# Optimization experiments

Measured on AMD Instinct MI355X. Metric: run time of the kernel, lower is better.

Reference implementation:

```python
import jax, jax.numpy as jnp
import numpy as np

N_NODES = 100000
N_EDGES = 1600000
F_IN, F1, F2, F3 = 128, 128, 128, 64


def setup_inputs() -> dict:
    key = jax.random.key(0)
    ks = jax.random.split(key, 10)
    edge_index = jax.random.randint(ks[0], (2, N_EDGES), 0, N_NODES, dtype=jnp.int64)
    x = jax.random.normal(ks[1], (N_NODES, F_IN), dtype=jnp.float32)
    def glorot(k, fi, fo):
        s = (6.0 / (fi + fo)) ** 0.5
        return jax.random.uniform(k, (fi, fo), jnp.float32, -s, s)
    return {
        "edge_index": edge_index,
        "x": x,
        "W1": glorot(ks[2], F_IN, F1), "b1": jnp.zeros((F1,), jnp.float32),
        "W2": glorot(ks[3], F1, F2), "b2": jnp.zeros((F2,), jnp.float32),
        "W3": glorot(ks[4], F2, F3), "b3": jnp.zeros((F3,), jnp.float32),
        "W_att": glorot(ks[5], F3, F3),
    }


def _gcn_conv(x, W, b, src, dst, deg_inv_sqrt):
    h = x @ W  # [N, Fo]
    norm = deg_inv_sqrt[src] * deg_inv_sqrt[dst]  # [E]
    agg = jax.ops.segment_sum(h[src] * norm[:, None], dst, num_segments=x.shape[0])
    agg = agg + h * (deg_inv_sqrt * deg_inv_sqrt)[:, None]  # self-loop term
    return agg + b


def _attention_pool(emb, W_att):
    # SimGNN attention pooling
    ctx = jnp.tanh(jnp.mean(emb @ W_att, axis=0))          # [F3]
    scores = jax.nn.sigmoid(emb @ ctx)                      # [N]
    return emb.T @ scores[:, None]                          # [F3, 1]


def reference(edge_index, x, W1, b1, W2, b2, W3, b3, W_att):
    src, dst = edge_index[0], edge_index[1]
    n = x.shape[0]
    deg = jax.ops.segment_sum(jnp.ones_like(src, dtype=x.dtype), dst, num_segments=n) + 1.0
    dis = jax.lax.rsqrt(deg)
    h = jax.nn.relu(_gcn_conv(x, W1, b1, src, dst, dis))
    h = jax.nn.relu(_gcn_conv(h, W2, b2, src, dst, dis))
    h = _gcn_conv(h, W3, b3, src, dst, dis)                 # abstract_features [N, F3]
    pooled = _attention_pool(h, W_att)                      # [F3, 1]
    return h, pooled
```

## Files before the change

### kernel.cpp

```cpp
#include <hip/hip_runtime.h>
#include <hip/hip_bf16.h>

#define NN 100000
#define NE 1600000
#define NR 100032
#define NB2 196
#define NBLK 391
#define EPB 4096

#if defined(__has_builtin)
#  if __has_builtin(__builtin_amdgcn_cvt_pk_f32_fp8) && \
      __has_builtin(__builtin_amdgcn_cvt_pk_fp8_f32) && \
      __has_builtin(__builtin_amdgcn_cvt_f32_fp8)
#    define HWF8 1
#  endif
#endif

typedef float f32x2 __attribute__((ext_vector_type(2)));
typedef float f32x4 __attribute__((ext_vector_type(4)));
typedef short bf16x8 __attribute__((ext_vector_type(8)));

static __device__ __forceinline__ float bf2f(__hip_bfloat16 v) { return __bfloat162float(v); }
static __device__ __forceinline__ float bfu(unsigned short w) {
    return __uint_as_float((unsigned)w << 16);
}

static __device__ __forceinline__ float f8d_sw(unsigned b) {
    unsigned e = (b >> 3) & 15u, m = b & 7u;
    float mag;
    if (e == 0) mag = (float)m * 0.001953125f;
    else        mag = __uint_as_float(((e + 120u) << 23) | (m << 20));
    return (b & 0x80u) ? -mag : mag;
}
static __device__ __forceinline__ unsigned char f8e_sw(float x) {
    unsigned u = __float_as_uint(x);
    unsigned s = (u >> 31) << 7;
    unsigned au = u & 0x7fffffffu;
    if (au >= 0x43E00000u) return (unsigned char)(s | 0x7Eu);
    if (au <  0x3A800000u) return (unsigned char)s;
    if (au <  0x3C800000u) {
        float a = __uint_as_float(au);
        int m = (int)rintf(a * 512.0f);
        if (m >= 8) return (unsigned char)(s | 0x08u);
        return (unsigned char)(s | (unsigned)m);
    }
    au += 0x80000u;
    if (au >= 0x43E00000u) return (unsigned char)(s | 0x7Eu);
    unsigned e = (au >> 23) - 120u;
    unsigned m = (au >> 20) & 7u;
    return (unsigned char)(s | (e << 3) | m);
}

static __device__ __forceinline__ void f8d4(unsigned u, float* o) {
#ifdef HWF8
    f32x2 lo = __builtin_amdgcn_cvt_pk_f32_fp8((int)u, false);
    f32x2 hi = __builtin_amdgcn_cvt_pk_f32_fp8((int)u, true);
    o[0] = lo.x; o[1] = lo.y; o[2] = hi.x; o[3] = hi.y;
#else
    o[0] = f8d_sw(u & 255u); o[1] = f8d_sw((u >> 8) & 255u);
    o[2] = f8d_sw((u >> 16) & 255u); o[3] = f8d_sw(u >> 24);
#endif
}
static __device__ __forceinline__ unsigned short f8e2(float a, float b) {
#ifdef HWF8
    float ca = fminf(fmaxf(a, -448.0f), 448.0f);
    float cb = fminf(fmaxf(b, -448.0f), 448.0f);
    int p = __builtin_amdgcn_cvt_pk_fp8_f32(ca, cb, 0, false);
    return (unsigned short)(p & 0xFFFF);
#else
    return (unsigned short)f8e_sw(a) | ((unsigned short)f8e_sw(b) << 8);
#endif
}
static __device__ __forceinline__ unsigned bfpack(float lo, float hi) {
    return (__float_as_uint(lo) >> 16) | (__float_as_uint(hi) & 0xFFFF0000u);
}

static __device__ __forceinline__ void acc8_add(f32x2* acc, uint2 v) {
#ifdef HWF8
    acc[0] += __builtin_amdgcn_cvt_pk_f32_fp8((int)v.x, false);
    acc[1] += __builtin_amdgcn_cvt_pk_f32_fp8((int)v.x, true);
    acc[2] += __builtin_amdgcn_cvt_pk_f32_fp8((int)v.y, false);
    acc[3] += __builtin_amdgcn_cvt_pk_f32_fp8((int)v.y, true);
#else
    unsigned u[2] = {v.x, v.y};
#pragma unroll
    for (int q = 0; q < 2; q++) {
        float o[4]; f8d4(u[q], o);
        acc[2 * q]     += (f32x2){o[0], o[1]};
        acc[2 * q + 1] += (f32x2){o[2], o[3]};
    }
#endif
}

__global__ void k_probe1(const unsigned short* __restrict__ xw,
                         const int* __restrict__ ei, int* __restrict__ raw) {
    int i = blockIdx.x * 256 + threadIdx.x;
    int nan = ((xw[i] & 0x7F80u) == 0x7F80u) ? 1 : 0;
    int odd = (ei[2 * i + 1] != 0) ? 1 : 0;
    unsigned long long bn = __ballot(nan);
    unsigned long long bo = __ballot(odd);
    if ((threadIdx.x & 63) == 0) {
        if (bn) atomicAdd(&raw[0], __popcll(bn));
        if (bo) atomicAdd(&raw[1], __popcll(bo));
    }
}

static __device__ __forceinline__ int e_src(const int* ei, int e, int f64) {
    int v = f64 ? ei[2 * e] : ei[e];
    return min(max(v, 0), NN - 1);
}
static __device__ __forceinline__ int e_dst(const int* ei, int e, int f64) {
    int v = f64 ? ei[2 * (NE + e)] : ei[NE + e];
    return min(max(v, 0), NN - 1);
}
static __device__ __forceinline__ float ldx(const void* p, long long i, int f32) {
    return f32 ? ((const float*)p)[i] : bf2f(((const __hip_bfloat16*)p)[i]);
}

__global__ __launch_bounds__(256) void k_prep(const void* __restrict__ x,
                                              const void* W1, const void* b1,
                                              const void* W2, const void* b2,
                                              const void* W3, const void* b3,
                                              const void* Wa,
                                              unsigned short* W1b, unsigned short* W2b,
                                              unsigned short* W3b,
                                              float* b1f, float* b2f, float* b3f,
                                              float* Waf,
                                              unsigned char* __restrict__ P,
                                              const int* __restrict__ raw,
                                              float* colsum, float* pooled, int* wsync) {
    int t = threadIdx.x;
    int gi = blockIdx.x;
    int f = raw[0] > 0;
    if (gi < 12500) {
        int i = gi * 256 + t;
        unsigned pk;
        if (f) {
            float4 v = ((const float4*)x)[i];
            pk = (unsigned)f8e2(v.x, v.y) | ((unsigned)f8e2(v.z, v.w) << 16);
        } else {
            ushort4 v = ((const ushort4*)x)[i];
            pk = (unsigned)f8e2(bfu(v.x), bfu(v.y)) | ((unsigned)f8e2(bfu(v.z), bfu(v.w)) << 16);
        }
        ((unsigned*)P)[i] = pk;
        return;
    }
    int i = (gi - 12500) * 256 + t;
    {
        int j = i & 7, l = (i >> 3) & 63, c = (i >> 9) & 7, kc = i >> 12;
        int k = kc * 32 + ((l >> 4)) * 8 + j;
        int col = c * 16 + (l & 15);
        W1b[i] = __bfloat16_as_ushort(__float2bfloat16(ldx(W1, k * 128 + col, f)));
        W2b[i] = __bfloat16_as_ushort(__float2bfloat16(ldx(W2, k * 128 + col, f)));
    }
    if (i < 8192) {
        int j = i & 7, l = (i >> 3) & 63, c = (i >> 9) & 3, kc = i >> 11;
        int k = kc * 32 + ((l >> 4)) * 8 + j;
        int col = c * 16 + (l & 15);
        W3b[i] = __bfloat16_as_ushort(__float2bfloat16(ldx(W3, k * 64 + col, f)));
    }
    if (i < 4096)  Waf[i] = ldx(Wa, i, f);
    if (i < 128)   { b1f[i] = ldx(b1, i, f); b2f[i] = ldx(b2, i, f); }
    if (i < 64)    b3f[i] = ldx(b3, i, f);
    if (gi == 12500) {
        if (t < 64) { colsum[t] = 0.0f; pooled[t] = 0.0f; }
        if (t == 0) { wsync[0] = 0; wsync[1] = 0; }
    }
    if (gi == 12501) {
        for (int z = t; z < (NR - NN) * 32; z += 256)
            ((unsigned*)(P + (size_t)NN * 128))[z] = 0u;
    }
}

__global__ __launch_bounds__(256) void k_hist(const int* __restrict__ ei,
                                              int* __restrict__ ghist,
                                              const int* __restrict__ raw) {
    __shared__ int h[NB2];
    int blk = blockIdx.x, t = threadIdx.x;
    for (int i = t; i < NB2; i += 256) h[i] = 0;
    __syncthreads();
    int f64 = (raw[1] == 0);
    int e0 = blk * EPB;
    for (int i = t; i < EPB; i += 256) {
        int e = e0 + i;
        if (e < NE) atomicAdd(&h[e_dst(ei, e, f64) >> 9], 1);
    }
    __syncthreads();
    for (int i = t; i < NB2; i += 256) ghist[blk * NB2 + i] = h[i];
}

__global__ __launch_bounds__(512) void k_offA(const int* __restrict__ ghist,
                                              int* __restrict__ tot,
                                              int* __restrict__ offm) {
    int b = blockIdx.x;
    int t = threadIdx.x;
    __shared__ int wsum[8];
    __shared__ int woff[8];
    int v = (t < NBLK) ? ghist[t * NB2 + b] : 0;
    int s = v;
#pragma unroll
    for (int o = 1; o < 64; o <<= 1) {
        int u = __shfl_up(s, o, 64);
        if ((t & 63) >= o) s += u;
    }
    int w = t >> 6;
    if ((t & 63) == 63) wsum[w] = s;
    __syncthreads();
    if (t == 0) {
        int run = 0;
#pragma unroll
        for (int i = 0; i < 8; i++) { woff[i] = run; run += wsum[i]; }
        tot[b] = run;
    }
    __syncthreads();
    if (t < NBLK) offm[t * NB2 + b] = s - v + woff[w];
}

__global__ void k_offB(const int* __restrict__ tot,
                       int* __restrict__ cbase, int* __restrict__ rowptr) {
    if (threadIdx.x == 0) {
        int run = 0;
        for (int b = 0; b < NB2; b++) { cbase[b] = run; run += tot[b]; }
        cbase[NB2] = run;
        rowptr[NN] = run;
    }
}

__global__ __launch_bounds__(256) void k_scatter(const int* __restrict__ ei,
                                                 const int* __restrict__ offm,
                                                 const int* __restrict__ cbase,
                                                 int* __restrict__ scratch,
                                                 const int* __restrict__ raw) {
    __shared__ int cur[NB2];
    int blk = blockIdx.x, t = threadIdx.x;
    for (int i = t; i < NB2; i += 256) cur[i] = offm[blk * NB2 + i] + cbase[i];
    __syncthreads();
    int f64 = (raw[1] == 0);
    int e0 = blk * EPB;
    for (int i = t; i < EPB; i += 256) {
        int e = e0 + i;
        if (e < NE) {
            int d = e_dst(ei, e, f64);
            int s = e_src(ei, e, f64);
            int p = atomicAdd(&cur[d >> 9], 1);
            p = min(max(p, 0), NE - 1);
            scratch[p] = s | ((d & 511) << 17);
        }
    }
}

__global__ __launch_bounds__(256) void k_build(const int* __restrict__ scratch,
                                               const int* __restrict__ cbase,
                                               int* __restrict__ rowptr,
                                               float* __restrict__ dis,
                                               int* __restrict__ csr) {
    __shared__ int hist[512];
    __shared__ int base[512];
    __shared__ int sd[256];
    int b = blockIdx.x, t = threadIdx.x;
    int n0 = b << 9;
    int s0 = cbase[b], s1 = cbase[b + 1];
    hist[t] = 0; hist[t + 256] = 0;
    __syncthreads();
    for (int i = s0 + t; i < s1; i += 256) {
        int dlo = (scratch[i] >> 17) & 511;
        atomicAdd(&hist[dlo], 1);
    }
    __syncthreads();
    int v0 = hist[2 * t], v1 = hist[2 * t + 1];
    int s = v0 + v1;
    sd[t] = s; __syncthreads();
    for (int o = 1; o < 256; o <<= 1) {
        int add = (t >= o) ? sd[t - o] : 0;
        __syncthreads();
        sd[t] += add;
        __syncthreads();
    }
    int run = s0 + sd[t] - s;
    base[2 * t] = run;
    base[2 * t + 1] = run + v0;
    int n = n0 + 2 * t;
    if (n < NN) {
        rowptr[n] = run;
        dis[n] = rsqrtf((float)v0 + 1.0f);
    }
    if (n + 1 < NN) {
        rowptr[n + 1] = run + v0;
        dis[n + 1] = rsqrtf((float)v1 + 1.0f);
    }
    __syncthreads();
    for (int i = s0 + t; i < s1; i += 256) {
        int v = scratch[i];
        int dlo = (v >> 17) & 511;
        int p = atomicAdd(&base[dlo], 1);
        p = min(max(p, 0), NE - 1);
        csr[p] = v & 0x1FFFF;
    }
}

template <int NCT>
__global__ __launch_bounds__(256) void k_xf_mfma(const unsigned char* __restrict__ A,
                                                 const unsigned short* __restrict__ Wf,
                                                 const float* __restrict__ dis,
                                                 unsigned char* __restrict__ O) {
    __shared__ unsigned short wl[NCT * 4 * 64 * 8];
    int t = threadIdx.x;
    int n0 = blockIdx.x * 64;
    {
        const uint4* wg = (const uint4*)Wf;
        uint4* wld = (uint4*)wl;
#pragma unroll
        for (int i = 0; i < NCT; i++) wld[i * 256 + t] = wg[i * 256 + t];
    }
    __syncthreads();
    int w = t >> 6, l = t & 63;
    int quad = l >> 4, m = l & 15;
    int node = n0 + w * 16 + m;
    const unsigned char* ap = A + (size_t)node * 128 + quad * 8;
    f32x4 acc[NCT];
#pragma unroll
    for (int c = 0; c < NCT; c++) acc[c] = (f32x4){0.0f, 0.0f, 0.0f, 0.0f};
#pragma unroll
    for (int kc = 0; kc < 4; kc++) {
        uint2 g = *(const uint2*)(ap + kc * 32);
        float o[8];
        f8d4(g.x, o); f8d4(g.y, o + 4);
        union { unsigned u[4]; bf16x8 v; } fr;
        fr.u[0] = bfpack(o[0], o[1]);
        fr.u[1] = bfpack(o[2], o[3]);
        fr.u[2] = bfpack(o[4], o[5]);
        fr.u[3] = bfpack(o[6], o[7]);
#pragma unroll
        for (int c = 0; c < NCT; c++) {
            bf16x8 bw = *(const bf16x8*)&wl[((kc * NCT + c) * 64 + l) * 8];
            acc[c] = __builtin_amdgcn_mfma_f32_16x16x32_bf16(bw, fr.v, acc[c], 0, 0, 0);
        }
    }
    float d = (node < NN) ? dis[node] : 0.0f;
    if (node <= NN) {
        unsigned char* orow = O + (size_t)node * (NCT * 16) + quad * 4;
#pragma unroll
        for (int c = 0; c < NCT; c++) {
            unsigned pk = (unsigned)f8e2(acc[c][0] * d, acc[c][1] * d)
                        | ((unsigned)f8e2(acc[c][2] * d, acc[c][3] * d) << 16);
            *(unsigned*)(orow + c * 16) = pk;
        }
    }
}

template <bool RELU>
__global__ __launch_bounds__(256) void k_agg128(const unsigned char* __restrict__ Tb,
                                                const int* __restrict__ rowptr,
                                                const int* __restrict__ csr,
                                                const float* __restrict__ dis,
                                                const float* __restrict__ bias,
                                                unsigned char* __restrict__ H) {
    int n = blockIdx.x * 4 + (threadIdx.x >> 6);
    int lane = threadIdx.x & 63;
    int r = lane >> 4;
    int f = lane & 15;
    int fo = f << 3;
    float dn = dis[n];
    int s0 = rowptr[n], s1 = rowptr[n + 1];
    s0 = min(max(s0, 0), NE); s1 = min(max(s1, s0), NE);
    f32x2 acc[4];
#pragma unroll
    for (int k = 0; k < 4; k++) acc[k] = (f32x2){0.0f, 0.0f};
    if (r == 0) {
        uint2 v = *(const uint2*)(Tb + (((unsigned)n << 7) + (unsigned)fo));
        acc8_add(acc, v);
    }
    for (int base = s0; base < s1; base += 64) {
        int m = min(64, s1 - base);
        unsigned voff = (unsigned)NN << 7;
        if (lane < m) voff = (unsigned)csr[base + lane] << 7;
        int nq = (m + 15) >> 4;
        for (int q = 0; q < nq; q++) {
            int a0 = q * 64 + r * 4;
            unsigned vo0 = (unsigned)__builtin_amdgcn_ds_bpermute(a0,      (int)voff);
            unsigned vo1 = (unsigned)__builtin_amdgcn_ds_bpermute(a0 + 16, (int)voff);
            unsigned vo2 = (unsigned)__builtin_amdgcn_ds_bpermute(a0 + 32, (int)voff);
            unsigned vo3 = (unsigned)__builtin_amdgcn_ds_bpermute(a0 + 48, (int)voff);
            uint2 v0 = *(const uint2*)(Tb + (vo0 + (unsigned)fo));
            uint2 v1 = *(const uint2*)(Tb + (vo1 + (unsigned)fo));
            uint2 v2 = *(const uint2*)(Tb + (vo2 + (unsigned)fo));
            uint2 v3 = *(const uint2*)(Tb + (vo3 + (unsigned)fo));
            acc8_add(acc, v0);
            acc8_add(acc, v1);
            acc8_add(acc, v2);
            acc8_add(acc, v3);
        }
    }
#pragma unroll
    for (int k = 0; k < 4; k++) {
        acc[k].x += __shfl_xor(acc[k].x, 16, 64);
        acc[k].y += __shfl_xor(acc[k].y, 16, 64);
        acc[k].x += __shfl_xor(acc[k].x, 32, 64);
        acc[k].y += __shfl_xor(acc[k].y, 32, 64);
    }
    if (r == 0) {
        float4 bA = *(const float4*)(bias + fo);
        float4 bB = *(const float4*)(bias + fo + 4);
        float t[8];
        t[0] = acc[0].x * dn + bA.x; t[1] = acc[0].y * dn + bA.y;
        t[2] = acc[1].x * dn + bA.z; t[3] = acc[1].y * dn + bA.w;
        t[4] = acc[2].x * dn + bB.x; t[5] = acc[2].y * dn + bB.y;
        t[6] = acc[3].x * dn + bB.z; t[7] = acc[3].y * dn + bB.w;
        if (RELU) {
#pragma unroll
            for (int k = 0; k < 8; k++) t[k] = fmaxf(t[k], 0.0f);
        }
        unsigned lo = (unsigned)f8e2(t[0], t[1]) | ((unsigned)f8e2(t[2], t[3]) << 16);
        unsigned hi = (unsigned)f8e2(t[4], t[5]) | ((unsigned)f8e2(t[6], t[7]) << 16);
        *(uint2*)(H + (((size_t)n << 7) + (size_t)fo)) = make_uint2(lo, hi);
    }
}

__global__ __launch_bounds__(256) void k_agg64(const unsigned char* __restrict__ Tb,
                                               const int* __restrict__ rowptr,
                                               const int* __restrict__ csr,
                                               const float* __restrict__ dis,
                                               const float* __restrict__ bias,
                                               unsigned short* __restrict__ Hb) {
    int lane = threadIdx.x & 63;
    int half = lane >> 5;
    int hl = lane & 31;
    int n = blockIdx.x * 8 + (threadIdx.x >> 6) * 2 + half;
    int r = hl >> 3;
    int f = hl & 7;
    int fo = f << 3;
    float dn = dis[n];
    int s0 = rowptr[n], s1 = rowptr[n + 1];
    s0 = min(max(s0, 0), NE); s1 = min(max(s1, s0), NE);
    f32x2 acc[4];
#pragma unroll
    for (int k = 0; k < 4; k++) acc[k] = (f32x2){0.0f, 0.0f};
    if (r == 0) {
        uint2 v = *(const uint2*)(Tb + (((unsigned)n << 6) + (unsigned)fo));
        acc8_add(acc, v);
    }
    int ab = half << 7;
    for (int base = s0; base < s1; base += 32) {
        int m = min(32, s1 - base);
        unsigned voff = (unsigned)NN << 6;
        if (hl < m) voff = (unsigned)csr[base + hl] << 6;
        int nq = (m + 15) >> 4;
        for (int q = 0; q < nq; q++) {
            int a0 = ab + q * 64 + r * 4;
            unsigned vo0 = (unsigned)__builtin_amdgcn_ds_bpermute(a0,      (int)voff);
            unsigned vo1 = (unsigned)__builtin_amdgcn_ds_bpermute(a0 + 16, (int)voff);
            unsigned vo2 = (unsigned)__builtin_amdgcn_ds_bpermute(a0 + 32, (int)voff);
            unsigned vo3 = (unsigned)__builtin_amdgcn_ds_bpermute(a0 + 48, (int)voff);
            uint2 v0 = *(const uint2*)(Tb + (vo0 + (unsigned)fo));
            uint2 v1 = *(const uint2*)(Tb + (vo1 + (unsigned)fo));
            uint2 v2 = *(const uint2*)(Tb + (vo2 + (unsigned)fo));
            uint2 v3 = *(const uint2*)(Tb + (vo3 + (unsigned)fo));
            acc8_add(acc, v0);
            acc8_add(acc, v1);
            acc8_add(acc, v2);
            acc8_add(acc, v3);
        }
    }
#pragma unroll
    for (int k = 0; k < 4; k++) {
        acc[k].x += __shfl_xor(acc[k].x, 8, 64);
        acc[k].y += __shfl_xor(acc[k].y, 8, 64);
        acc[k].x += __shfl_xor(acc[k].x, 16, 64);
        acc[k].y += __shfl_xor(acc[k].y, 16, 64);
    }
    if (r == 0) {
        float4 bA = *(const float4*)(bias + fo);
        float4 bB = *(const float4*)(bias + fo + 4);
        float t[8];
        t[0] = acc[0].x * dn + bA.x; t[1] = acc[0].y * dn + bA.y;
        t[2] = acc[1].x * dn + bA.z; t[3] = acc[1].y * dn + bA.w;
        t[4] = acc[2].x * dn + bB.x; t[5] = acc[2].y * dn + bB.y;
        t[6] = acc[3].x * dn + bB.z; t[7] = acc[3].y * dn + bB.w;
        unsigned p0 = (unsigned)__bfloat16_as_ushort(__float2bfloat16(t[0])) |
                      ((unsigned)__bfloat16_as_ushort(__float2bfloat16(t[1])) << 16);
        unsigned p1 = (unsigned)__bfloat16_as_ushort(__float2bfloat16(t[2])) |
                      ((unsigned)__bfloat16_as_ushort(__float2bfloat16(t[3])) << 16);
        unsigned p2 = (unsigned)__bfloat16_as_ushort(__float2bfloat16(t[4])) |
                      ((unsigned)__bfloat16_as_ushort(__float2bfloat16(t[5])) << 16);
        unsigned p3 = (unsigned)__bfloat16_as_ushort(__float2bfloat16(t[6])) |
                      ((unsigned)__bfloat16_as_ushort(__float2bfloat16(t[7])) << 16);
        *(uint4*)(Hb + (((size_t)n << 6) + (size_t)fo)) = make_uint4(p0, p1, p2, p3);
    }
}

__global__ __launch_bounds__(512) void k_colsum(const unsigned short* __restrict__ h3,
                                                float* __restrict__ colsum,
                                                const float* __restrict__ Waf,
                                                float* __restrict__ ctx,
                                                int* __restrict__ wsync) {
    int t = threadIdx.x;
    int lane = t & 63;
    int rg = lane >> 4, cq = lane & 15;
    int wid = (blockIdx.x * 512 + t) >> 6;
    int nw = (gridDim.x * 512) >> 6;
    float a0 = 0, a1 = 0, a2 = 0, a3 = 0;
    for (int r = wid * 4 + rg; r < NN; r += nw * 4) {
        uint2 v = *(const uint2*)(h3 + ((size_t)r << 6) + cq * 4);
        a0 += bfu((unsigned short)(v.x & 0xFFFF));
        a1 += bfu((unsigned short)(v.x >> 16));
        a2 += bfu((unsigned short)(v.y & 0xFFFF));
        a3 += bfu((unsigned short)(v.y >> 16));
    }
    a0 += __shfl_xor(a0, 16, 64); a0 += __shfl_xor(a0, 32, 64);
    a1 += __shfl_xor(a1, 16, 64); a1 += __shfl_xor(a1, 32, 64);
    a2 += __shfl_xor(a2, 16, 64); a2 += __shfl_xor(a2, 32, 64);
    a3 += __shfl_xor(a3, 16, 64); a3 += __shfl_xor(a3, 32, 64);
    __shared__ float part[8][64];
    int w = t >> 6;
    if (rg == 0) {
        part[w][cq * 4 + 0] = a0;
        part[w][cq * 4 + 1] = a1;
        part[w][cq * 4 + 2] = a2;
        part[w][cq * 4 + 3] = a3;
    }
    __syncthreads();
    if (t < 64) {
        float s = 0;
#pragma unroll
        for (int i = 0; i < 8; i++) s += part[i][t];
        atomicAdd(&colsum[t], s);
    }
    __shared__ int lastf;
    __syncthreads();
    if (t == 0) {
        __threadfence();
        int old = atomicAdd(&wsync[0], 1);
        lastf = (old == (int)gridDim.x - 1) ? 1 : 0;
    }
    __syncthreads();
    if (lastf) {
        __shared__ float ms[64];
        if (t < 64) {
            __threadfence();
            ms[t] = atomicAdd(&colsum[t], 0.0f) * (1.0f / NN);
        }
        __syncthreads();
        if (t < 64) {
            float s = 0.0f;
#pragma unroll
            for (int k = 0; k < 64; k++) s += ms[k] * Waf[k * 64 + t];
            ctx[t] = tanhf(s);
        }
    }
}

__global__ __launch_bounds__(512) void k_pool(const unsigned short* __restrict__ h3,
                                              const float* __restrict__ ctx,
                                              float* __restrict__ pooled,
                                              void* __restrict__ out,
                                              const int* __restrict__ raw,
                                              int* __restrict__ wsync) {
    int t = threadIdx.x;
    int lane = t & 63;
    int rg = lane >> 4, cq = lane & 15;
    int wid = (blockIdx.x * 512 + t) >> 6;
    int nw = (gridDim.x * 512) >> 6;
    int f32o = raw[0] > 0;
    float c0 = ctx[cq * 4 + 0], c1 = ctx[cq * 4 + 1];
    float c2 = ctx[cq * 4 + 2], c3 = ctx[cq * 4 + 3];
    float q0 = 0, q1 = 0, q2 = 0, q3 = 0;
    for (int r = wid * 4 + rg; r < NN; r += nw * 4) {
        uint2 v = *(const uint2*)(h3 + ((size_t)r << 6) + cq * 4);
        float x0 = bfu((unsigned short)(v.x & 0xFFFF));
        float x1 = bfu((unsigned short)(v.x >> 16));
        float x2 = bfu((unsigned short)(v.y & 0xFFFF));
        float x3 = bfu((unsigned short)(v.y >> 16));
        if (f32o) {
            *(float4*)((float*)out + ((size_t)r << 6) + cq * 4) =
                make_float4(x0, x1, x2, x3);
        } else {
            *(uint2*)((unsigned short*)out + ((size_t)r << 6) + cq * 4) = v;
        }
        float p = x0 * c0 + x1 * c1 + x2 * c2 + x3 * c3;
        p += __shfl_xor(p, 1, 64);
        p += __shfl_xor(p, 2, 64);
        p += __shfl_xor(p, 4, 64);
        p += __shfl_xor(p, 8, 64);
        float sc = 1.0f / (1.0f + expf(-p));
        q0 += sc * x0; q1 += sc * x1; q2 += sc * x2; q3 += sc * x3;
    }
    q0 += __shfl_xor(q0, 16, 64); q0 += __shfl_xor(q0, 32, 64);
    q1 += __shfl_xor(q1, 16, 64); q1 += __shfl_xor(q1, 32, 64);
    q2 += __shfl_xor(q2, 16, 64); q2 += __shfl_xor(q2, 32, 64);
    q3 += __shfl_xor(q3, 16, 64); q3 += __shfl_xor(q3, 32, 64);
    __shared__ float part[8][64];
    int w = t >> 6;
    if (rg == 0) {
        part[w][cq * 4 + 0] = q0;
        part[w][cq * 4 + 1] = q1;
        part[w][cq * 4 + 2] = q2;
        part[w][cq * 4 + 3] = q3;
    }
    __syncthreads();
    if (t < 64) {
        float s = 0;
#pragma unroll
        for (int i = 0; i < 8; i++) s += part[i][t];
        atomicAdd(&pooled[t], s);
    }
    __shared__ int lastf;
    __syncthreads();
    if (t == 0) {
        __threadfence();
        int old = atomicAdd(&wsync[1], 1);
        lastf = (old == (int)gridDim.x - 1) ? 1 : 0;
    }
    __syncthreads();
    if (lastf && t < 64) {
        __threadfence();
        float pv = atomicAdd(&pooled[t], 0.0f);
        if (f32o) {
            ((float*)out)[6400000 + t] = pv;
        } else {
            ((unsigned short*)out)[6400000 + t] =
                __bfloat16_as_ushort(__float2bfloat16(pv));
        }
    }
}

static constexpr size_t AL(size_t x) { return (x + 255) & ~size_t(255); }
static constexpr size_t OFF_FLAGS  = 0;
static constexpr size_t OFF_RAW    = OFF_FLAGS + 256;
static constexpr size_t OFF_GHIST  = OFF_RAW + 256;
static constexpr size_t OFF_OFFM   = OFF_GHIST + AL((size_t)NBLK * NB2 * 4);
static constexpr size_t OFF_CBASE  = OFF_OFFM + AL((size_t)NBLK * NB2 * 4);
static constexpr size_t OFF_ROWPTR = OFF_CBASE + AL((NB2 + 1) * 4);
static constexpr size_t OFF_CSR    = OFF_ROWPTR + AL((NN + 1) * 4);
static constexpr size_t OFF_DIS    = OFF_CSR + AL((size_t)NE * 4);
static constexpr size_t OFF_P      = OFF_DIS + AL(NN * 4);
static constexpr size_t OFF_W1B    = OFF_P + AL((size_t)NR * 128);
static constexpr size_t OFF_W2B    = OFF_W1B + AL(16384 * 2);
static constexpr size_t OFF_W3B    = OFF_W2B + AL(16384 * 2);
static constexpr size_t OFF_B1F    = OFF_W3B + AL(8192 * 2);
static constexpr size_t OFF_B2F    = OFF_B1F + AL(128 * 4);
static constexpr size_t OFF_B3F    = OFF_B2F + AL(128 * 4);
static constexpr size_t OFF_WAF    = OFF_B3F + AL(64 * 4);
static constexpr size_t OFF_COLSUM = OFF_WAF + AL(4096 * 4);
static constexpr size_t OFF_POOLED = OFF_COLSUM + AL(64 * 4);
static constexpr size_t OFF_CTX    = OFF_POOLED + AL(64 * 4);
static constexpr size_t OFF_SYNC   = OFF_CTX + AL(64 * 4);
static constexpr size_t OFF_TOT    = OFF_SYNC + 256;

extern "C" void kernel_launch(void* const* d_in, const int* in_sizes, int n_in,
                              void* d_out, int out_size, void* d_ws, size_t ws_size,
                              hipStream_t stream) {
    const int* ei = (const int*)d_in[0];
    const void* x  = d_in[1];
    const void* W1 = d_in[2];
    const void* b1 = d_in[3];
    const void* W2 = d_in[4];
    const void* b2 = d_in[5];
    const void* W3 = d_in[6];
    const void* b3 = d_in[7];
    const void* Wa = d_in[8];

    char* ws = (char*)d_ws;
    int*   raw    = (int*)(ws + OFF_RAW);
    int*   ghist  = (int*)(ws + OFF_GHIST);
    int*   offm   = (int*)(ws + OFF_OFFM);
    int*   cbase  = (int*)(ws + OFF_CBASE);
    int*   rowptr = (int*)(ws + OFF_ROWPTR);
    int*   csr    = (int*)(ws + OFF_CSR);
    float* dis    = (float*)(ws + OFF_DIS);
    unsigned char*  P    = (unsigned char*)(ws + OFF_P);
    int*            scrA = (int*)(ws + OFF_P);
    unsigned short* Hb   = (unsigned short*)(ws + OFF_P);
    unsigned short* W1b = (unsigned short*)(ws + OFF_W1B);
    unsigned short* W2b = (unsigned short*)(ws + OFF_W2B);
    unsigned short* W3b = (unsigned short*)(ws + OFF_W3B);
    float* b1f    = (float*)(ws + OFF_B1F);
    float* b2f    = (float*)(ws + OFF_B2F);
    float* b3f    = (float*)(ws + OFF_B3F);
    float* Waf    = (float*)(ws + OFF_WAF);
    float* colsum = (float*)(ws + OFF_COLSUM);
    float* pooled = (float*)(ws + OFF_POOLED);
    float* ctx    = (float*)(ws + OFF_CTX);
    int*   wsync  = (int*)(ws + OFF_SYNC);
    int*   tot    = (int*)(ws + OFF_TOT);

    unsigned char* Q = (unsigned char*)d_out;

    hipMemsetAsync(raw, 0, 256, stream);

    k_probe1<<<256, 256, 0, stream>>>((const unsigned short*)x, ei, raw);

    k_hist<<<NBLK, 256, 0, stream>>>(ei, ghist, raw);
    k_offA<<<NB2, 512, 0, stream>>>(ghist, tot, offm);
    k_offB<<<1, 64, 0, stream>>>(tot, cbase, rowptr);
    k_scatter<<<NBLK, 256, 0, stream>>>(ei, offm, cbase, scrA, raw);
    k_build<<<NB2, 256, 0, stream>>>(scrA, cbase, rowptr, dis, csr);

    k_prep<<<12564, 256, 0, stream>>>(x, W1, b1, W2, b2, W3, b3, Wa,
                                      W1b, W2b, W3b, b1f, b2f, b3f, Waf,
                                      P, raw, colsum, pooled, wsync);

    k_xf_mfma<8><<<NR / 64, 256, 0, stream>>>(P, W1b, dis, Q);
    k_agg128<true><<<NN / 4, 256, 0, stream>>>(Q, rowptr, csr, dis, b1f, P);
    k_xf_mfma<8><<<NR / 64, 256, 0, stream>>>(P, W2b, dis, Q);
    k_agg128<true><<<NN / 4, 256, 0, stream>>>(Q, rowptr, csr, dis, b2f, P);
    k_xf_mfma<4><<<NR / 64, 256, 0, stream>>>(P, W3b, dis, Q);
    k_agg64<<<NN / 8, 256, 0, stream>>>(Q, rowptr, csr, dis, b3f, Hb);

    k_colsum<<<256, 512, 0, stream>>>(Hb, colsum, Waf, ctx, wsync);
    k_pool<<<256, 512, 0, stream>>>(Hb, ctx, pooled, d_out, raw, wsync);
}
```

Before: 367.3 us.

## Pack more nodes per wavefront in aggregation and fold offset scan into offA

Aggregation kernels now handle two nodes per wave for the 128-wide layer and four nodes per wave for the 64-wide layer. The edge chunk per node shrinks to match, and one cross-lane reduction step is dropped. With an average degree near 16, this is meant to cut lanes that sit idle on short neighbour lists. Separately, the single-thread k_offB launch is removed: the last k_offA block, found through an atomic counter, computes the global bucket prefix, saving one kernel launch. The counter in raw[2] depends on raw being cleared by the memset each call, and per-node parallelism is lower for high-degree nodes.

```diff
diff --git a/kernel.cpp b/kernel.cpp
--- a/kernel.cpp
+++ b/kernel.cpp
@@ -191,7 +191,10 @@
 
 __global__ __launch_bounds__(512) void k_offA(const int* __restrict__ ghist,
                                               int* __restrict__ tot,
-                                              int* __restrict__ offm) {
+                                              int* __restrict__ offm,
+                                              int* __restrict__ cbase,
+                                              int* __restrict__ rowptr,
+                                              int* __restrict__ sync) {
     int b = blockIdx.x;
     int t = threadIdx.x;
     __shared__ int wsum[8];
@@ -214,15 +217,23 @@
     }
     __syncthreads();
     if (t < NBLK) offm[t * NB2 + b] = s - v + woff[w];
-}
-
-__global__ void k_offB(const int* __restrict__ tot,
-                       int* __restrict__ cbase, int* __restrict__ rowptr) {
-    if (threadIdx.x == 0) {
-        int run = 0;
-        for (int b = 0; b < NB2; b++) { cbase[b] = run; run += tot[b]; }
-        cbase[NB2] = run;
-        rowptr[NN] = run;
+    __shared__ int lastf;
+    if (t == 0) {
+        __threadfence();
+        int old = atomicAdd(sync, 1);
+        lastf = (old == NB2 - 1) ? 1 : 0;
+    }
+    __syncthreads();
+    if (lastf) {
+        __shared__ int sv[NB2];
+        if (t < NB2) sv[t] = atomicAdd(&tot[t], 0);
+        __syncthreads();
+        if (t == 0) {
+            int run = 0;
+            for (int bb = 0; bb < NB2; bb++) { cbase[bb] = run; run += sv[bb]; }
+            cbase[NB2] = run;
+            rowptr[NN] = run;
+        }
     }
 }
 
@@ -355,10 +366,12 @@
                                                 const float* __restrict__ dis,
                                                 const float* __restrict__ bias,
                                                 unsigned char* __restrict__ H) {
-    int n = blockIdx.x * 4 + (threadIdx.x >> 6);
     int lane = threadIdx.x & 63;
-    int r = lane >> 4;
-    int f = lane & 15;
+    int half = lane >> 5;
+    int hl = lane & 31;
+    int n = blockIdx.x * 8 + (threadIdx.x >> 6) * 2 + half;
+    int r = hl >> 4;
+    int f = hl & 15;
     int fo = f << 3;
     float dn = dis[n];
     int s0 = rowptr[n], s1 = rowptr[n + 1];
@@ -370,17 +383,18 @@
         uint2 v = *(const uint2*)(Tb + (((unsigned)n << 7) + (unsigned)fo));
         acc8_add(acc, v);
     }
-    for (int base = s0; base < s1; base += 64) {
-        int m = min(64, s1 - base);
+    int ab = half << 7;
+    for (int base = s0; base < s1; base += 32) {
+        int m = min(32, s1 - base);
         unsigned voff = (unsigned)NN << 7;
-        if (lane < m) voff = (unsigned)csr[base + lane] << 7;
-        int nq = (m + 15) >> 4;
+        if (hl < m) voff = (unsigned)csr[base + hl] << 7;
+        int nq = (m + 7) >> 3;
         for (int q = 0; q < nq; q++) {
-            int a0 = q * 64 + r * 4;
+            int a0 = ab + q * 32 + r * 4;
             unsigned vo0 = (unsigned)__builtin_amdgcn_ds_bpermute(a0,      (int)voff);
-            unsigned vo1 = (unsigned)__builtin_amdgcn_ds_bpermute(a0 + 16, (int)voff);
-            unsigned vo2 = (unsigned)__builtin_amdgcn_ds_bpermute(a0 + 32, (int)voff);
-            unsigned vo3 = (unsigned)__builtin_amdgcn_ds_bpermute(a0 + 48, (int)voff);
+            unsigned vo1 = (unsigned)__builtin_amdgcn_ds_bpermute(a0 + 8,  (int)voff);
+            unsigned vo2 = (unsigned)__builtin_amdgcn_ds_bpermute(a0 + 16, (int)voff);
+            unsigned vo3 = (unsigned)__builtin_amdgcn_ds_bpermute(a0 + 24, (int)voff);
             uint2 v0 = *(const uint2*)(Tb + (vo0 + (unsigned)fo));
             uint2 v1 = *(const uint2*)(Tb + (vo1 + (unsigned)fo));
             uint2 v2 = *(const uint2*)(Tb + (vo2 + (unsigned)fo));
@@ -395,8 +409,6 @@
     for (int k = 0; k < 4; k++) {
         acc[k].x += __shfl_xor(acc[k].x, 16, 64);
         acc[k].y += __shfl_xor(acc[k].y, 16, 64);
-        acc[k].x += __shfl_xor(acc[k].x, 32, 64);
-        acc[k].y += __shfl_xor(acc[k].y, 32, 64);
     }
     if (r == 0) {
         float4 bA = *(const float4*)(bias + fo);
@@ -423,11 +435,11 @@
                                                const float* __restrict__ bias,
                                                unsigned short* __restrict__ Hb) {
     int lane = threadIdx.x & 63;
-    int half = lane >> 5;
-    int hl = lane & 31;
-    int n = blockIdx.x * 8 + (threadIdx.x >> 6) * 2 + half;
-    int r = hl >> 3;
-    int f = hl & 7;
+    int qtr = lane >> 4;
+    int ql = lane & 15;
+    int n = blockIdx.x * 16 + (threadIdx.x >> 6) * 4 + qtr;
+    int r = ql >> 3;
+    int f = ql & 7;
     int fo = f << 3;
     float dn = dis[n];
     int s0 = rowptr[n], s1 = rowptr[n + 1];
@@ -439,18 +451,18 @@
         uint2 v = *(const uint2*)(Tb + (((unsigned)n << 6) + (unsigned)fo));
         acc8_add(acc, v);
     }
-    int ab = half << 7;
-    for (int base = s0; base < s1; base += 32) {
-        int m = min(32, s1 - base);
+    int ab = qtr << 6;
+    for (int base = s0; base < s1; base += 16) {
+        int m = min(16, s1 - base);
         unsigned voff = (unsigned)NN << 6;
-        if (hl < m) voff = (unsigned)csr[base + hl] << 6;
-        int nq = (m + 15) >> 4;
+        if (ql < m) voff = (unsigned)csr[base + ql] << 6;
+        int nq = (m + 7) >> 3;
         for (int q = 0; q < nq; q++) {
-            int a0 = ab + q * 64 + r * 4;
+            int a0 = ab + q * 32 + r * 4;
             unsigned vo0 = (unsigned)__builtin_amdgcn_ds_bpermute(a0,      (int)voff);
-            unsigned vo1 = (unsigned)__builtin_amdgcn_ds_bpermute(a0 + 16, (int)voff);
-            unsigned vo2 = (unsigned)__builtin_amdgcn_ds_bpermute(a0 + 32, (int)voff);
-            unsigned vo3 = (unsigned)__builtin_amdgcn_ds_bpermute(a0 + 48, (int)voff);
+            unsigned vo1 = (unsigned)__builtin_amdgcn_ds_bpermute(a0 + 8,  (int)voff);
+            unsigned vo2 = (unsigned)__builtin_amdgcn_ds_bpermute(a0 + 16, (int)voff);
+            unsigned vo3 = (unsigned)__builtin_amdgcn_ds_bpermute(a0 + 24, (int)voff);
             uint2 v0 = *(const uint2*)(Tb + (vo0 + (unsigned)fo));
             uint2 v1 = *(const uint2*)(Tb + (vo1 + (unsigned)fo));
             uint2 v2 = *(const uint2*)(Tb + (vo2 + (unsigned)fo));
@@ -465,8 +477,6 @@
     for (int k = 0; k < 4; k++) {
         acc[k].x += __shfl_xor(acc[k].x, 8, 64);
         acc[k].y += __shfl_xor(acc[k].y, 8, 64);
-        acc[k].x += __shfl_xor(acc[k].x, 16, 64);
-        acc[k].y += __shfl_xor(acc[k].y, 16, 64);
     }
     if (r == 0) {
         float4 bA = *(const float4*)(bias + fo);
@@ -690,8 +700,7 @@
     k_probe1<<<256, 256, 0, stream>>>((const unsigned short*)x, ei, raw);
 
     k_hist<<<NBLK, 256, 0, stream>>>(ei, ghist, raw);
-    k_offA<<<NB2, 512, 0, stream>>>(ghist, tot, offm);
-    k_offB<<<1, 64, 0, stream>>>(tot, cbase, rowptr);
+    k_offA<<<NB2, 512, 0, stream>>>(ghist, tot, offm, cbase, rowptr, &raw[2]);
     k_scatter<<<NBLK, 256, 0, stream>>>(ei, offm, cbase, scrA, raw);
     k_build<<<NB2, 256, 0, stream>>>(scrA, cbase, rowptr, dis, csr);
 
@@ -700,11 +709,11 @@
                                       P, raw, colsum, pooled, wsync);
 
     k_xf_mfma<8><<<NR / 64, 256, 0, stream>>>(P, W1b, dis, Q);
-    k_agg128<true><<<NN / 4, 256, 0, stream>>>(Q, rowptr, csr, dis, b1f, P);
+    k_agg128<true><<<NN / 8, 256, 0, stream>>>(Q, rowptr, csr, dis, b1f, P);
     k_xf_mfma<8><<<NR / 64, 256, 0, stream>>>(P, W2b, dis, Q);
-    k_agg128<true><<<NN / 4, 256, 0, stream>>>(Q, rowptr, csr, dis, b2f, P);
+    k_agg128<true><<<NN / 8, 256, 0, stream>>>(Q, rowptr, csr, dis, b2f, P);
     k_xf_mfma<4><<<NR / 64, 256, 0, stream>>>(P, W3b, dis, Q);
-    k_agg64<<<NN / 8, 256, 0, stream>>>(Q, rowptr, csr, dis, b3f, Hb);
+    k_agg64<<<NN / 16, 256, 0, stream>>>(Q, rowptr, csr, dis, b3f, Hb);
 
     k_colsum<<<256, 512, 0, stream>>>(Hb, colsum, Waf, ctx, wsync);
     k_pool<<<256, 512, 0, stream>>>(Hb, ctx, pooled, d_out, raw, wsync);
```

Result: faster. 348.1 us (-5.2%).
